# Performance work log

Measured on AMD Instinct MI355X. Metric: run time of the kernel, lower is better.

The kernel has to match this reference:

```python
import jax, jax.numpy as jnp
import numpy as np

N = 4096        # n_locations
D_MODEL = 512
H, D_K, D_V = 4, 128, 256


def setup_inputs() -> dict:
    key = jax.random.key(0)
    ks = jax.random.split(key, 7)
    s = 0.02
    return {
        "Q": jax.random.normal(ks[0], (N, D_MODEL), dtype=jnp.float32),
        "K": jax.random.normal(ks[1], (N, D_MODEL), dtype=jnp.float32),
        "V": jax.random.normal(ks[2], (N, D_MODEL), dtype=jnp.float32),
        "Wq": jax.random.normal(ks[3], (H, D_MODEL, D_K), dtype=jnp.float32) * s,
        "Wk": jax.random.normal(ks[4], (H, D_MODEL, D_K), dtype=jnp.float32) * s,
        "Wv": jax.random.normal(ks[5], (H, D_MODEL, D_V), dtype=jnp.float32) * s,
        "Wo": jax.random.normal(ks[6], (D_MODEL, H * D_V), dtype=jnp.float32) * s,
    }


def reference(Q, K, V, Wq, Wk, Wv, Wo):
    n = K.shape[0]
    # Batched per-head projections: [h, n, d_k] / [h, n, d_v]
    q = jnp.einsum('nd,hdk->hnk', Q, Wq)
    k = jnp.einsum('nd,hdk->hnk', K, Wk)
    v = jnp.einsum('nd,hdv->hnv', V, Wv)
    # NOTE: original scales by sqrt(n_locations) (K.size(0)), not sqrt(d_k)
    scores = jnp.einsum('hqk,hnk->hqn', q, k) / jnp.sqrt(jnp.asarray(n, q.dtype))
    weights = jax.nn.softmax(scores, axis=-1)          # [h, n, n]
    heads = jnp.einsum('hqn,hnv->hqv', weights, v)      # [h, n, d_v]
    # concat heads along feature dim: [n, h*d_v]
    x = jnp.transpose(heads, (1, 0, 2)).reshape(heads.shape[1], -1)
    return x @ Wo.T                                     # [n, d_model]
```

## Files before the change

### kernel.cpp

```cpp
#include <hip/hip_runtime.h>
#include <hip/hip_bf16.h>
#include <type_traits>

typedef __hip_bfloat16 bf16;
typedef __attribute__((ext_vector_type(8))) short bf16x8;
typedef __attribute__((ext_vector_type(4))) float f32x4;

#define N_LOC 4096

__device__ __forceinline__ bf16 to_bf16(float f) { return __float2bfloat16(f); }

__device__ __forceinline__ void dma16(const bf16* g, bf16* l) {
  __builtin_amdgcn_global_load_lds((const __attribute__((address_space(1))) unsigned int*)g,
                                   (__attribute__((address_space(3))) unsigned int*)l, 16, 0, 0);
}

__global__ __launch_bounds__(256) void convert_all(const float* __restrict__ Q,
                                                   const float* __restrict__ K,
                                                   const float* __restrict__ V,
                                                   const float* __restrict__ Wo,
                                                   bf16* __restrict__ Qb, bf16* __restrict__ Kb,
                                                   bf16* __restrict__ Vb, bf16* __restrict__ Wob) {
  long i = ((long)blockIdx.x * 256 + threadIdx.x) * 8;
  const float* src;
  bf16* dst;
  long off;
  if (i < 2097152)      { src = Q;  dst = Qb;  off = i; }
  else if (i < 4194304) { src = K;  dst = Kb;  off = i - 2097152; }
  else if (i < 6291456) { src = V;  dst = Vb;  off = i - 4194304; }
  else                  { src = Wo; dst = Wob; off = i - 6291456; }
  float4 a = *(const float4*)&src[off];
  float4 b = *(const float4*)&src[off + 4];
  union { bf16 h[8]; bf16x8 v; } u;
  u.h[0] = to_bf16(a.x); u.h[1] = to_bf16(a.y); u.h[2] = to_bf16(a.z); u.h[3] = to_bf16(a.w);
  u.h[4] = to_bf16(b.x); u.h[5] = to_bf16(b.y); u.h[6] = to_bf16(b.z); u.h[7] = to_bf16(b.w);
  *(bf16x8*)&dst[off] = u.v;
}

__global__ __launch_bounds__(256) void pack_wt(const float* __restrict__ Wq,
                                               const float* __restrict__ Wk,
                                               const float* __restrict__ Wv,
                                               bf16* __restrict__ oq, bf16* __restrict__ ok,
                                               bf16* __restrict__ ov) {
  int z = blockIdx.z;
  const float* W = (z == 0) ? Wq : (z == 1) ? Wk : Wv;
  bf16* out = (z == 0) ? oq : (z == 1) ? ok : ov;
  int DH = (z == 2) ? 256 : 128;
  int nt = DH >> 6;
  int y = blockIdx.y;
  if (y >= 4 * nt) return;
  int h = y / nt, tt = y - h * nt;
  int d0 = blockIdx.x * 64, t0 = tt * 64;
  __shared__ float tile[64][65];
  for (int i = threadIdx.x; i < 4096; i += 256) {
    int r = i >> 6, c = i & 63;
    tile[r][c] = W[((size_t)h * 512 + d0 + r) * DH + t0 + c];
  }
  __syncthreads();
  for (int i = threadIdx.x; i < 4096; i += 256) {
    int t = i >> 6, d = i & 63;
    out[((size_t)(h * DH + t0 + t)) * 512 + d0 + d] = to_bf16(tile[d][t]);
  }
}

template <typename OutT>
__device__ __forceinline__ void gemm128_body(const bf16* __restrict__ A,
                                             const bf16* __restrict__ Bt,
                                             OutT* __restrict__ C, int M, int N, int K,
                                             int m0, int n0, bf16* As, bf16* Bs) {
  int tid = threadIdx.x;
  int lane = tid & 63, w = tid >> 6;
  int quad = lane >> 4, l16 = lane & 15;
  int wm = (w >> 1) * 64, wn = (w & 1) * 64;
  int srow = lane >> 3;
  int sG = (lane & 7) ^ srow;

  f32x4 acc[4][4] = {};
  for (int k0 = 0; k0 < K; k0 += 64) {
#pragma unroll
    for (int j = 0; j < 4; j++) {
      int rg = 4 * j + w;
      dma16(&A[(long)(m0 + rg * 8 + srow) * K + k0 + sG * 8], &As[rg * 512]);
      dma16(&Bt[(long)(n0 + rg * 8 + srow) * K + k0 + sG * 8], &Bs[rg * 512]);
    }
    __syncthreads();
#pragma unroll
    for (int kk = 0; kk < 2; kk++) {
      bf16x8 af[4], bfr[4];
#pragma unroll
      for (int i = 0; i < 4; i++) {
        int r = wm + i * 16 + l16;
        af[i] = *(const bf16x8*)&As[r * 64 + (((kk * 4 + quad) ^ r) & 7) * 8];
      }
#pragma unroll
      for (int j = 0; j < 4; j++) {
        int r = wn + j * 16 + l16;
        bfr[j] = *(const bf16x8*)&Bs[r * 64 + (((kk * 4 + quad) ^ r) & 7) * 8];
      }
#pragma unroll
      for (int i = 0; i < 4; i++)
#pragma unroll
        for (int j = 0; j < 4; j++)
          acc[i][j] = __builtin_amdgcn_mfma_f32_16x16x32_bf16(af[i], bfr[j], acc[i][j], 0, 0, 0);
    }
    __syncthreads();
  }
#pragma unroll
  for (int i = 0; i < 4; i++)
#pragma unroll
    for (int j = 0; j < 4; j++)
#pragma unroll
      for (int r = 0; r < 4; r++) {
        long row = m0 + wm + i * 16 + quad * 4 + r;
        long col = n0 + wn + j * 16 + l16;
        if constexpr (std::is_same<OutT, bf16>::value)
          C[row * N + col] = to_bf16(acc[i][j][r]);
        else
          C[row * N + col] = acc[i][j][r];
      }
}

__global__ __launch_bounds__(256) void proj_gemm(const bf16* __restrict__ QKVb,
                                                 const bf16* __restrict__ Wt,
                                                 bf16* __restrict__ Cout) {
  int z = blockIdx.z;
  int N = (z == 2) ? 1024 : 512;
  if ((int)(blockIdx.y * 128) >= N) return;
  __shared__ __align__(16) bf16 As[128 * 64];
  __shared__ __align__(16) bf16 Bs[128 * 64];
  const bf16* A = QKVb + (size_t)z * 2097152;
  const bf16* Bt = Wt + ((z == 2) ? (size_t)524288 : (size_t)z * 262144);
  bf16* C = Cout + (size_t)z * 2097152;
  gemm128_body<bf16>(A, Bt, C, 4096, N, 512, blockIdx.x * 128, blockIdx.y * 128, As, Bs);
}

__global__ __launch_bounds__(256) void out_gemm(const bf16* __restrict__ xin,
                                                const bf16* __restrict__ Wob,
                                                float* __restrict__ outp) {
  __shared__ __align__(16) bf16 As[128 * 64];
  __shared__ __align__(16) bf16 Bs[128 * 64];
  gemm128_body<float>(xin, Wob, outp, 4096, 512, 1024, blockIdx.x * 128, blockIdx.y * 128, As, Bs);
}

__global__ __launch_bounds__(256) void transpose_bf16(const bf16* __restrict__ in,
                                                      bf16* __restrict__ out, int R, int Cc) {
  long T = (long)blockIdx.x * 256 + threadIdx.x;
  long nrb = (long)(R >> 3);
  long rb = T % nrb;
  long cb = T / nrb;
  union { bf16 h[8]; bf16x8 v; } a[8], b[8];
#pragma unroll
  for (int i = 0; i < 8; i++) a[i].v = *(const bf16x8*)&in[(rb * 8 + i) * Cc + cb * 8];
#pragma unroll
  for (int j = 0; j < 8; j++) {
#pragma unroll
    for (int i = 0; i < 8; i++) b[j].h[i] = a[i].h[j];
    *(bf16x8*)&out[(cb * 8 + j) * R + rb * 8] = b[j].v;
  }
}

__global__ __launch_bounds__(512, 2) void attn(const bf16* __restrict__ qb,
                                               const bf16* __restrict__ kb,
                                               const bf16* __restrict__ vT,
                                               bf16* __restrict__ x) {
  __shared__ __align__(16) bf16 kt[2][64 * 128];
  __shared__ __align__(16) bf16 vt[2][256 * 64];
  __shared__ __align__(16) bf16 pt[64 * 72];
  __shared__ float Lrow[64];

  const int head = blockIdx.x & 3;
  const int q0 = (blockIdx.x >> 2) * 64;
  const int tid = threadIdx.x;
  const int lane = tid & 63, w = tid >> 6;
  const int quad = lane >> 4, l16 = lane & 15;
  const int cd = w & 3;
  const int g = w >> 2;

  bf16x8 onesf;
  {
    union { bf16 h[8]; bf16x8 v; } u;
    bf16 one = to_bf16(1.0f), zero = to_bf16(0.0f);
#pragma unroll
    for (int j = 0; j < 8; j++) u.h[j] = (l16 == 0) ? one : zero;
    onesf = u.v;
  }

  bf16x8 qf[2][4];
#pragma unroll
  for (int i = 0; i < 2; i++) {
    const bf16* qrow = &qb[(size_t)(q0 + g * 32 + i * 16 + l16) * 512 + head * 128];
#pragma unroll
    for (int kk = 0; kk < 4; kk++) qf[i][kk] = *(const bf16x8*)&qrow[kk * 32 + quad * 8];
  }

  f32x4 oacc[2][4] = {};
  f32x4 oL[2] = {};
  const float scale = 1.0f / 64.0f;

  auto stage = [&](int b, int key0) {
#pragma unroll
    for (int t2 = 0; t2 < 2; t2++) {
      int j = 2 * w + t2;
      int r = 4 * j + (lane >> 4);
      int p = lane & 15;
      int G = (p & 8) | ((p ^ r) & 7);
      dma16(&kb[(size_t)(key0 + r) * 512 + head * 128 + G * 8], &kt[b][j * 512]);
    }
#pragma unroll
    for (int t2 = 0; t2 < 4; t2++) {
      int j = 4 * w + t2;
      int r = 8 * j + (lane >> 3);
      int p = lane & 7;
      int G = (p ^ r) & 7;
      dma16(&vT[(size_t)(head * 256 + r) * 4096 + key0 + G * 8], &vt[b][j * 512]);
    }
  };

  stage(0, 0);
  asm volatile("" ::: "memory");
  int cur = 0;

  for (int t = 0; t < 64; ++t) {
    if (t < 63) {
      stage(cur ^ 1, (t + 1) * 64);
      asm volatile("s_waitcnt vmcnt(6)" ::: "memory");
    } else {
      asm volatile("s_waitcnt vmcnt(0)" ::: "memory");
    }
    __builtin_amdgcn_s_barrier();
    asm volatile("" ::: "memory");

    const bf16* ktc = kt[cur];
    f32x4 sacc[2] = {};
#pragma unroll
    for (int kk = 0; kk < 4; kk++) {
      int R = cd * 16 + l16;
      int G = kk * 4 + quad;
      bf16x8 kf = *(const bf16x8*)&ktc[R * 128 + (((G ^ R) & 7) | (G & 8)) * 8];
      sacc[0] = __builtin_amdgcn_mfma_f32_16x16x32_bf16(qf[0][kk], kf, sacc[0], 0, 0, 0);
      sacc[1] = __builtin_amdgcn_mfma_f32_16x16x32_bf16(qf[1][kk], kf, sacc[1], 0, 0, 0);
    }
#pragma unroll
    for (int i = 0; i < 2; i++)
#pragma unroll
      for (int r = 0; r < 4; r++)
        pt[(g * 32 + i * 16 + quad * 4 + r) * 72 + cd * 16 + l16] =
            to_bf16(__expf(sacc[i][r] * scale));
    asm volatile("s_waitcnt lgkmcnt(0)" ::: "memory");
    __builtin_amdgcn_s_barrier();
    asm volatile("" ::: "memory");

    const bf16* vtc = vt[cur];
#pragma unroll
    for (int kk = 0; kk < 2; kk++) {
      bf16x8 pf[2];
#pragma unroll
      for (int i = 0; i < 2; i++)
        pf[i] = *(const bf16x8*)&pt[(g * 32 + i * 16 + l16) * 72 + kk * 32 + quad * 8];
#pragma unroll
      for (int c = 0; c < 4; c++) {
        int R = cd * 64 + c * 16 + l16;
        int G = kk * 4 + quad;
        bf16x8 vf = *(const bf16x8*)&vtc[R * 64 + ((G ^ R) & 7) * 8];
#pragma unroll
        for (int i = 0; i < 2; i++)
          oacc[i][c] = __builtin_amdgcn_mfma_f32_16x16x32_bf16(pf[i], vf, oacc[i][c], 0, 0, 0);
      }
      if (cd == 3) {
#pragma unroll
        for (int i = 0; i < 2; i++)
          oL[i] = __builtin_amdgcn_mfma_f32_16x16x32_bf16(pf[i], onesf, oL[i], 0, 0, 0);
      }
    }
    asm volatile("" ::: "memory");
    __builtin_amdgcn_s_barrier();
    asm volatile("" ::: "memory");
    cur ^= 1;
  }

  if (cd == 3 && l16 == 0) {
#pragma unroll
    for (int i = 0; i < 2; i++)
#pragma unroll
      for (int r = 0; r < 4; r++) Lrow[g * 32 + i * 16 + quad * 4 + r] = oL[i][r];
  }
  __syncthreads();

#pragma unroll
  for (int i = 0; i < 2; i++)
#pragma unroll
    for (int c = 0; c < 4; c++)
#pragma unroll
      for (int r = 0; r < 4; r++) {
        int row = g * 32 + i * 16 + quad * 4 + r;
        float v = oacc[i][c][r] / Lrow[row];
        x[(size_t)(q0 + row) * 1024 + head * 256 + cd * 64 + c * 16 + l16] = to_bf16(v);
      }
}

extern "C" void kernel_launch(void* const* d_in, const int* in_sizes, int n_in,
                              void* d_out, int out_size, void* d_ws, size_t ws_size,
                              hipStream_t stream) {
  const float* Q  = (const float*)d_in[0];
  const float* Km = (const float*)d_in[1];
  const float* V  = (const float*)d_in[2];
  const float* Wq = (const float*)d_in[3];
  const float* Wk = (const float*)d_in[4];
  const float* Wv = (const float*)d_in[5];
  const float* Wo = (const float*)d_in[6];
  float* out = (float*)d_out;

  bf16* ws  = (bf16*)d_ws;
  bf16* Qb  = ws;
  bf16* Kb  = Qb + 2097152;
  bf16* Vb  = Kb + 2097152;
  bf16* Wqt = Vb + 2097152;
  bf16* Wkt = Wqt + 262144;
  bf16* Wvt = Wkt + 262144;
  bf16* Wob = Wvt + 524288;
  bf16* qb  = Wob + 524288;
  bf16* kb  = qb + 2097152;
  bf16* vb  = kb + 2097152;
  bf16* vT  = vb + 4194304;
  bf16* x   = vT + 4194304;

  convert_all<<<3328, 256, 0, stream>>>(Q, Km, V, Wo, Qb, Kb, Vb, Wob);
  pack_wt<<<dim3(8, 16, 3), 256, 0, stream>>>(Wq, Wk, Wv, Wqt, Wkt, Wvt);

  proj_gemm<<<dim3(32, 8, 3), 256, 0, stream>>>(Qb, Wqt, qb);
  transpose_bf16<<<256, 256, 0, stream>>>(vb, vT, 4096, 1024);

  attn<<<256, 512, 0, stream>>>(qb, kb, vT, x);

  out_gemm<<<dim3(32, 4), 256, 0, stream>>>(x, Wob, out);
}
```

Baseline: 227.8 us.

## Fuse prep kernels, double-buffer GEMMs, fuse V transpose, split attention over d_v

Merges the convert and weight-pack kernels into one launch. Gives the GEMM body double-buffered LDS loads with explicit vmcnt waits. The V projection now writes its transposed output directly through an LDS epilogue, which removes the separate transpose kernel and the intermediate V buffer. Attention splits each head's d_v into two halves, doubling the grid to 512 blocks with higher occupancy bounds, at the cost of recomputing QK^T and exp twice per head. The output GEMM uses 64-wide N tiles for more blocks.

```diff
diff --git a/kernel.cpp b/kernel.cpp
--- a/kernel.cpp
+++ b/kernel.cpp
@@ -15,161 +15,198 @@
                                    (__attribute__((address_space(3))) unsigned int*)l, 16, 0, 0);
 }
 
-__global__ __launch_bounds__(256) void convert_all(const float* __restrict__ Q,
-                                                   const float* __restrict__ K,
-                                                   const float* __restrict__ V,
-                                                   const float* __restrict__ Wo,
-                                                   bf16* __restrict__ Qb, bf16* __restrict__ Kb,
-                                                   bf16* __restrict__ Vb, bf16* __restrict__ Wob) {
-  long i = ((long)blockIdx.x * 256 + threadIdx.x) * 8;
-  const float* src;
-  bf16* dst;
-  long off;
-  if (i < 2097152)      { src = Q;  dst = Qb;  off = i; }
-  else if (i < 4194304) { src = K;  dst = Kb;  off = i - 2097152; }
-  else if (i < 6291456) { src = V;  dst = Vb;  off = i - 4194304; }
-  else                  { src = Wo; dst = Wob; off = i - 6291456; }
-  float4 a = *(const float4*)&src[off];
-  float4 b = *(const float4*)&src[off + 4];
-  union { bf16 h[8]; bf16x8 v; } u;
-  u.h[0] = to_bf16(a.x); u.h[1] = to_bf16(a.y); u.h[2] = to_bf16(a.z); u.h[3] = to_bf16(a.w);
-  u.h[4] = to_bf16(b.x); u.h[5] = to_bf16(b.y); u.h[6] = to_bf16(b.z); u.h[7] = to_bf16(b.w);
-  *(bf16x8*)&dst[off] = u.v;
-}
-
-__global__ __launch_bounds__(256) void pack_wt(const float* __restrict__ Wq,
-                                               const float* __restrict__ Wk,
-                                               const float* __restrict__ Wv,
-                                               bf16* __restrict__ oq, bf16* __restrict__ ok,
-                                               bf16* __restrict__ ov) {
-  int z = blockIdx.z;
-  const float* W = (z == 0) ? Wq : (z == 1) ? Wk : Wv;
-  bf16* out = (z == 0) ? oq : (z == 1) ? ok : ov;
-  int DH = (z == 2) ? 256 : 128;
-  int nt = DH >> 6;
-  int y = blockIdx.y;
-  if (y >= 4 * nt) return;
-  int h = y / nt, tt = y - h * nt;
-  int d0 = blockIdx.x * 64, t0 = tt * 64;
+__global__ __launch_bounds__(256) void prep(const float* __restrict__ Q, const float* __restrict__ K,
+                                            const float* __restrict__ V, const float* __restrict__ Wo,
+                                            bf16* __restrict__ Qb, bf16* __restrict__ Kb,
+                                            bf16* __restrict__ Vb, bf16* __restrict__ Wob,
+                                            const float* __restrict__ Wq, const float* __restrict__ Wk,
+                                            const float* __restrict__ Wv,
+                                            bf16* __restrict__ oq, bf16* __restrict__ ok,
+                                            bf16* __restrict__ ov) {
   __shared__ float tile[64][65];
-  for (int i = threadIdx.x; i < 4096; i += 256) {
-    int r = i >> 6, c = i & 63;
-    tile[r][c] = W[((size_t)h * 512 + d0 + r) * DH + t0 + c];
-  }
-  __syncthreads();
-  for (int i = threadIdx.x; i < 4096; i += 256) {
-    int t = i >> 6, d = i & 63;
-    out[((size_t)(h * DH + t0 + t)) * 512 + d0 + d] = to_bf16(tile[d][t]);
-  }
-}
-
-template <typename OutT>
-__device__ __forceinline__ void gemm128_body(const bf16* __restrict__ A,
-                                             const bf16* __restrict__ Bt,
-                                             OutT* __restrict__ C, int M, int N, int K,
-                                             int m0, int n0, bf16* As, bf16* Bs) {
-  int tid = threadIdx.x;
-  int lane = tid & 63, w = tid >> 6;
+  if (blockIdx.x < 3328) {
+    long i = ((long)blockIdx.x * 256 + threadIdx.x) * 8;
+    const float* src;
+    bf16* dst;
+    long off;
+    if (i < 2097152)      { src = Q;  dst = Qb;  off = i; }
+    else if (i < 4194304) { src = K;  dst = Kb;  off = i - 2097152; }
+    else if (i < 6291456) { src = V;  dst = Vb;  off = i - 4194304; }
+    else                  { src = Wo; dst = Wob; off = i - 6291456; }
+    float4 a = *(const float4*)&src[off];
+    float4 b = *(const float4*)&src[off + 4];
+    union { bf16 h[8]; bf16x8 v; } u;
+    u.h[0] = to_bf16(a.x); u.h[1] = to_bf16(a.y); u.h[2] = to_bf16(a.z); u.h[3] = to_bf16(a.w);
+    u.h[4] = to_bf16(b.x); u.h[5] = to_bf16(b.y); u.h[6] = to_bf16(b.z); u.h[7] = to_bf16(b.w);
+    *(bf16x8*)&dst[off] = u.v;
+  } else {
+    int pid = blockIdx.x - 3328;
+    int z = pid >> 7;
+    int rem = pid & 127;
+    int xx = rem & 7, y = rem >> 3;
+    const float* W = (z == 0) ? Wq : (z == 1) ? Wk : Wv;
+    bf16* out = (z == 0) ? oq : (z == 1) ? ok : ov;
+    int DH = (z == 2) ? 256 : 128;
+    int nt = DH >> 6;
+    if (y >= 4 * nt) return;
+    int h = y / nt, tt = y - h * nt;
+    int d0 = xx * 64, t0 = tt * 64;
+    for (int i = threadIdx.x; i < 4096; i += 256) {
+      int r = i >> 6, c = i & 63;
+      tile[r][c] = W[((size_t)h * 512 + d0 + r) * DH + t0 + c];
+    }
+    __syncthreads();
+    for (int i = threadIdx.x; i < 4096; i += 256) {
+      int t = i >> 6, d = i & 63;
+      out[((size_t)(h * DH + t0 + t)) * 512 + d0 + d] = to_bf16(tile[d][t]);
+    }
+  }
+}
+
+template <int BN, int MODE, typename OutT>
+__device__ __forceinline__ void gemm_body(const bf16* __restrict__ A, const bf16* __restrict__ Bt,
+                                          OutT* __restrict__ C, int N, int K, int m0, int n0,
+                                          bf16* sm) {
+  constexpr int WN = BN / 2, JN = WN / 16, NB = BN / 32;
+  int tid = threadIdx.x, lane = tid & 63, w = tid >> 6;
   int quad = lane >> 4, l16 = lane & 15;
-  int wm = (w >> 1) * 64, wn = (w & 1) * 64;
+  int wm = (w >> 1) * 64, wn = (w & 1) * WN;
   int srow = lane >> 3;
   int sG = (lane & 7) ^ srow;
 
-  f32x4 acc[4][4] = {};
-  for (int k0 = 0; k0 < K; k0 += 64) {
-#pragma unroll
-    for (int j = 0; j < 4; j++) {
-      int rg = 4 * j + w;
-      dma16(&A[(long)(m0 + rg * 8 + srow) * K + k0 + sG * 8], &As[rg * 512]);
-      dma16(&Bt[(long)(n0 + rg * 8 + srow) * K + k0 + sG * 8], &Bs[rg * 512]);
-    }
-    __syncthreads();
+  bf16* Asb[2] = { sm, sm + 8192 };
+  bf16* Bsb[2] = { sm + 16384, sm + 16384 + BN * 64 };
+
+  const bf16* ga[4];
+  const bf16* gb[NB];
+#pragma unroll
+  for (int j = 0; j < 4; j++) ga[j] = A + (long)(m0 + (4 * j + w) * 8 + srow) * K + sG * 8;
+#pragma unroll
+  for (int j = 0; j < NB; j++) gb[j] = Bt + (long)(n0 + (4 * j + w) * 8 + srow) * K + sG * 8;
+
+  auto stage = [&](int b) {
+#pragma unroll
+    for (int j = 0; j < 4; j++) { dma16(ga[j], &Asb[b][(4 * j + w) * 512]); ga[j] += 64; }
+#pragma unroll
+    for (int j = 0; j < NB; j++) { dma16(gb[j], &Bsb[b][(4 * j + w) * 512]); gb[j] += 64; }
+  };
+
+  f32x4 acc[4][JN] = {};
+  stage(0);
+  asm volatile("" ::: "memory");
+  int cur = 0;
+  const int NK = K >> 6;
+  for (int s = 0; s < NK; ++s) {
+    if (s + 1 < NK) {
+      stage(cur ^ 1);
+      if constexpr (NB == 4) asm volatile("s_waitcnt vmcnt(8)" ::: "memory");
+      else                   asm volatile("s_waitcnt vmcnt(6)" ::: "memory");
+    } else {
+      asm volatile("s_waitcnt vmcnt(0)" ::: "memory");
+    }
+    __builtin_amdgcn_s_barrier();
+    asm volatile("" ::: "memory");
+    const bf16* Ac = Asb[cur];
+    const bf16* Bc = Bsb[cur];
 #pragma unroll
     for (int kk = 0; kk < 2; kk++) {
-      bf16x8 af[4], bfr[4];
+      bf16x8 af[4], bfr[JN];
 #pragma unroll
       for (int i = 0; i < 4; i++) {
         int r = wm + i * 16 + l16;
-        af[i] = *(const bf16x8*)&As[r * 64 + (((kk * 4 + quad) ^ r) & 7) * 8];
-      }
-#pragma unroll
-      for (int j = 0; j < 4; j++) {
+        af[i] = *(const bf16x8*)&Ac[r * 64 + (((kk * 4 + quad) ^ r) & 7) * 8];
+      }
+#pragma unroll
+      for (int j = 0; j < JN; j++) {
         int r = wn + j * 16 + l16;
-        bfr[j] = *(const bf16x8*)&Bs[r * 64 + (((kk * 4 + quad) ^ r) & 7) * 8];
+        bfr[j] = *(const bf16x8*)&Bc[r * 64 + (((kk * 4 + quad) ^ r) & 7) * 8];
       }
 #pragma unroll
       for (int i = 0; i < 4; i++)
 #pragma unroll
-        for (int j = 0; j < 4; j++)
+        for (int j = 0; j < JN; j++)
           acc[i][j] = __builtin_amdgcn_mfma_f32_16x16x32_bf16(af[i], bfr[j], acc[i][j], 0, 0, 0);
     }
+    asm volatile("" ::: "memory");
+    __builtin_amdgcn_s_barrier();
+    asm volatile("" ::: "memory");
+    cur ^= 1;
+  }
+
+  if constexpr (MODE == 2) {
+    bf16* tp = sm;
+#pragma unroll
+    for (int i = 0; i < 4; i++)
+#pragma unroll
+      for (int j = 0; j < JN; j++)
+#pragma unroll
+        for (int r = 0; r < 4; r++)
+          tp[(wn + j * 16 + l16) * 136 + wm + i * 16 + quad * 4 + r] = to_bf16(acc[i][j][r]);
     __syncthreads();
-  }
-#pragma unroll
-  for (int i = 0; i < 4; i++)
-#pragma unroll
-    for (int j = 0; j < 4; j++)
-#pragma unroll
-      for (int r = 0; r < 4; r++) {
-        long row = m0 + wm + i * 16 + quad * 4 + r;
-        long col = n0 + wn + j * 16 + l16;
-        if constexpr (std::is_same<OutT, bf16>::value)
-          C[row * N + col] = to_bf16(acc[i][j][r]);
-        else
-          C[row * N + col] = acc[i][j][r];
-      }
+#pragma unroll
+    for (int it = 0; it < 8; ++it) {
+      int idx = it * 256 + tid;
+      int rown = idx >> 4, c8 = (idx & 15) * 8;
+      *(bf16x8*)&C[(size_t)(n0 + rown) * 4096 + m0 + c8] = *(const bf16x8*)&tp[rown * 136 + c8];
+    }
+  } else {
+#pragma unroll
+    for (int i = 0; i < 4; i++)
+#pragma unroll
+      for (int j = 0; j < JN; j++)
+#pragma unroll
+        for (int r = 0; r < 4; r++) {
+          long row = m0 + wm + i * 16 + quad * 4 + r;
+          long col = n0 + wn + j * 16 + l16;
+          if constexpr (MODE == 0)
+            C[row * N + col] = to_bf16(acc[i][j][r]);
+          else
+            C[row * N + col] = acc[i][j][r];
+        }
+  }
 }
 
 __global__ __launch_bounds__(256) void proj_gemm(const bf16* __restrict__ QKVb,
                                                  const bf16* __restrict__ Wt,
-                                                 bf16* __restrict__ Cout) {
-  int z = blockIdx.z;
-  int N = (z == 2) ? 1024 : 512;
-  if ((int)(blockIdx.y * 128) >= N) return;
-  __shared__ __align__(16) bf16 As[128 * 64];
-  __shared__ __align__(16) bf16 Bs[128 * 64];
-  const bf16* A = QKVb + (size_t)z * 2097152;
-  const bf16* Bt = Wt + ((z == 2) ? (size_t)524288 : (size_t)z * 262144);
-  bf16* C = Cout + (size_t)z * 2097152;
-  gemm128_body<bf16>(A, Bt, C, 4096, N, 512, blockIdx.x * 128, blockIdx.y * 128, As, Bs);
+                                                 bf16* __restrict__ qkout,
+                                                 bf16* __restrict__ vTout) {
+  __shared__ __align__(16) bf16 sm[4 * 128 * 64];
+  int bid = blockIdx.x;
+  if (bid < 256) {
+    int z = bid >> 7;
+    int t = bid & 127;
+    int m0 = (t & 31) * 128, n0 = (t >> 5) * 128;
+    gemm_body<128, 0, bf16>(QKVb + (size_t)z * 2097152, Wt + (size_t)z * 262144,
+                            qkout + (size_t)z * 2097152, 512, 512, m0, n0, sm);
+  } else {
+    int t = bid - 256;
+    int m0 = (t & 31) * 128, n0 = (t >> 5) * 128;
+    gemm_body<128, 2, bf16>(QKVb + (size_t)2 * 2097152, Wt + (size_t)2 * 262144,
+                            vTout, 1024, 512, m0, n0, sm);
+  }
 }
 
 __global__ __launch_bounds__(256) void out_gemm(const bf16* __restrict__ xin,
                                                 const bf16* __restrict__ Wob,
                                                 float* __restrict__ outp) {
-  __shared__ __align__(16) bf16 As[128 * 64];
-  __shared__ __align__(16) bf16 Bs[128 * 64];
-  gemm128_body<float>(xin, Wob, outp, 4096, 512, 1024, blockIdx.x * 128, blockIdx.y * 128, As, Bs);
-}
-
-__global__ __launch_bounds__(256) void transpose_bf16(const bf16* __restrict__ in,
-                                                      bf16* __restrict__ out, int R, int Cc) {
-  long T = (long)blockIdx.x * 256 + threadIdx.x;
-  long nrb = (long)(R >> 3);
-  long rb = T % nrb;
-  long cb = T / nrb;
-  union { bf16 h[8]; bf16x8 v; } a[8], b[8];
-#pragma unroll
-  for (int i = 0; i < 8; i++) a[i].v = *(const bf16x8*)&in[(rb * 8 + i) * Cc + cb * 8];
-#pragma unroll
-  for (int j = 0; j < 8; j++) {
-#pragma unroll
-    for (int i = 0; i < 8; i++) b[j].h[i] = a[i].h[j];
-    *(bf16x8*)&out[(cb * 8 + j) * R + rb * 8] = b[j].v;
-  }
-}
-
-__global__ __launch_bounds__(512, 2) void attn(const bf16* __restrict__ qb,
+  __shared__ __align__(16) bf16 sm[2 * 128 * 64 + 2 * 64 * 64];
+  gemm_body<64, 1, float>(xin, Wob, outp, 512, 1024, blockIdx.x * 128, blockIdx.y * 64, sm);
+}
+
+__global__ __launch_bounds__(512, 4) void attn(const bf16* __restrict__ qb,
                                                const bf16* __restrict__ kb,
                                                const bf16* __restrict__ vT,
                                                bf16* __restrict__ x) {
   __shared__ __align__(16) bf16 kt[2][64 * 128];
-  __shared__ __align__(16) bf16 vt[2][256 * 64];
+  __shared__ __align__(16) bf16 vt[2][128 * 64];
   __shared__ __align__(16) bf16 pt[64 * 72];
   __shared__ float Lrow[64];
 
-  const int head = blockIdx.x & 3;
-  const int q0 = (blockIdx.x >> 2) * 64;
+  const int bid = blockIdx.x;
+  const int xcd = bid & 7;
+  const int head = xcd & 3;
+  const int dvh = xcd >> 2;
+  const int q0 = (bid >> 3) * 64;
   const int tid = threadIdx.x;
   const int lane = tid & 63, w = tid >> 6;
   const int quad = lane >> 4, l16 = lane & 15;
@@ -193,37 +230,45 @@
     for (int kk = 0; kk < 4; kk++) qf[i][kk] = *(const bf16x8*)&qrow[kk * 32 + quad * 8];
   }
 
-  f32x4 oacc[2][4] = {};
+  f32x4 oacc[2][2] = {};
   f32x4 oL[2] = {};
   const float scale = 1.0f / 64.0f;
 
-  auto stage = [&](int b, int key0) {
-#pragma unroll
-    for (int t2 = 0; t2 < 2; t2++) {
-      int j = 2 * w + t2;
-      int r = 4 * j + (lane >> 4);
-      int p = lane & 15;
-      int G = (p & 8) | ((p ^ r) & 7);
-      dma16(&kb[(size_t)(key0 + r) * 512 + head * 128 + G * 8], &kt[b][j * 512]);
-    }
-#pragma unroll
-    for (int t2 = 0; t2 < 4; t2++) {
-      int j = 4 * w + t2;
-      int r = 8 * j + (lane >> 3);
-      int p = lane & 7;
-      int G = (p ^ r) & 7;
-      dma16(&vT[(size_t)(head * 256 + r) * 4096 + key0 + G * 8], &vt[b][j * 512]);
-    }
-  };
-
-  stage(0, 0);
+  const int j0 = 2 * w, j1 = 2 * w + 1;
+  const bf16 *kp0, *kp1, *vp0, *vp1;
+  {
+    int r0 = 4 * j0 + (lane >> 4), r1 = 4 * j1 + (lane >> 4);
+    int p = lane & 15;
+    int G0 = (p & 8) | ((p ^ r0) & 7), G1 = (p & 8) | ((p ^ r1) & 7);
+    kp0 = kb + (size_t)r0 * 512 + head * 128 + G0 * 8;
+    kp1 = kb + (size_t)r1 * 512 + head * 128 + G1 * 8;
+  }
+  {
+    int r0 = 8 * j0 + (lane >> 3), r1 = 8 * j1 + (lane >> 3);
+    int p = lane & 7;
+    int G0 = (p ^ r0) & 7, G1 = (p ^ r1) & 7;
+    vp0 = vT + (size_t)(head * 256 + dvh * 128 + r0) * 4096 + G0 * 8;
+    vp1 = vT + (size_t)(head * 256 + dvh * 128 + r1) * 4096 + G1 * 8;
+  }
+
+#define STAGE(b)                                        \
+  do {                                                  \
+    dma16(kp0, &kt[b][j0 * 512]);                       \
+    dma16(kp1, &kt[b][j1 * 512]);                       \
+    dma16(vp0, &vt[b][j0 * 512]);                       \
+    dma16(vp1, &vt[b][j1 * 512]);                       \
+    kp0 += 64 * 512; kp1 += 64 * 512;                   \
+    vp0 += 64; vp1 += 64;                               \
+  } while (0)
+
+  STAGE(0);
   asm volatile("" ::: "memory");
   int cur = 0;
 
   for (int t = 0; t < 64; ++t) {
     if (t < 63) {
-      stage(cur ^ 1, (t + 1) * 64);
-      asm volatile("s_waitcnt vmcnt(6)" ::: "memory");
+      STAGE(cur ^ 1);
+      asm volatile("s_waitcnt vmcnt(4)" ::: "memory");
     } else {
       asm volatile("s_waitcnt vmcnt(0)" ::: "memory");
     }
@@ -258,8 +303,8 @@
       for (int i = 0; i < 2; i++)
         pf[i] = *(const bf16x8*)&pt[(g * 32 + i * 16 + l16) * 72 + kk * 32 + quad * 8];
 #pragma unroll
-      for (int c = 0; c < 4; c++) {
-        int R = cd * 64 + c * 16 + l16;
+      for (int c = 0; c < 2; c++) {
+        int R = cd * 32 + c * 16 + l16;
         int G = kk * 4 + quad;
         bf16x8 vf = *(const bf16x8*)&vtc[R * 64 + ((G ^ R) & 7) * 8];
 #pragma unroll
@@ -277,6 +322,7 @@
     asm volatile("" ::: "memory");
     cur ^= 1;
   }
+#undef STAGE
 
   if (cd == 3 && l16 == 0) {
 #pragma unroll
@@ -289,12 +335,13 @@
 #pragma unroll
   for (int i = 0; i < 2; i++)
 #pragma unroll
-    for (int c = 0; c < 4; c++)
+    for (int c = 0; c < 2; c++)
 #pragma unroll
       for (int r = 0; r < 4; r++) {
         int row = g * 32 + i * 16 + quad * 4 + r;
         float v = oacc[i][c][r] / Lrow[row];
-        x[(size_t)(q0 + row) * 1024 + head * 256 + cd * 64 + c * 16 + l16] = to_bf16(v);
+        x[(size_t)(q0 + row) * 1024 + head * 256 + dvh * 128 + cd * 32 + c * 16 + l16] =
+            to_bf16(v);
       }
 }
 
@@ -320,17 +367,14 @@
   bf16* Wob = Wvt + 524288;
   bf16* qb  = Wob + 524288;
   bf16* kb  = qb + 2097152;
-  bf16* vb  = kb + 2097152;
-  bf16* vT  = vb + 4194304;
+  bf16* vT  = kb + 2097152;
   bf16* x   = vT + 4194304;
 
-  convert_all<<<3328, 256, 0, stream>>>(Q, Km, V, Wo, Qb, Kb, Vb, Wob);
-  pack_wt<<<dim3(8, 16, 3), 256, 0, stream>>>(Wq, Wk, Wv, Wqt, Wkt, Wvt);
-
-  proj_gemm<<<dim3(32, 8, 3), 256, 0, stream>>>(Qb, Wqt, qb);
-  transpose_bf16<<<256, 256, 0, stream>>>(vb, vT, 4096, 1024);
-
-  attn<<<256, 512, 0, stream>>>(qb, kb, vT, x);
-
-  out_gemm<<<dim3(32, 4), 256, 0, stream>>>(x, Wob, out);
-}
+  prep<<<3712, 256, 0, stream>>>(Q, Km, V, Wo, Qb, Kb, Vb, Wob, Wq, Wk, Wv, Wqt, Wkt, Wvt);
+
+  proj_gemm<<<512, 256, 0, stream>>>(Qb, Wqt, qb, vT);
+
+  attn<<<512, 512, 0, stream>>>(qb, kb, vT, x);
+
+  out_gemm<<<dim3(32, 8), 256, 0, stream>>>(x, Wob, out);
+}
```

New measurement: 214.2 us. 6.0% less time.
